# Kernel tuning notes

Hardware: AMD Instinct MI355X
Metric: run time of the kernel (lower is better)

## Reference

```python
import jax, jax.numpy as jnp
import numpy as np

B, C, H, W = 4, 64, 160, 160
OUT, KH, KW = 64, 3, 3
STRIDE, PAD = 1, 1
K2 = KH * KW


def conv2d(x, w, b=None, stride=STRIDE, pad=PAD):
    y = jax.lax.conv_general_dilated(
        x, w, window_strides=(stride, stride),
        padding=[(pad, pad), (pad, pad)],
        dimension_numbers=("NCHW", "OIHW", "NCHW"))
    if b is not None:
        y = y + b[None, :, None, None]
    return y


def bilinear_gather(x, py, px):
    # x: [B,C,H,W]; py,px: [B,K2,Ho,Wo] float sampling positions
    Bq, Cq, Hq, Wq = x.shape
    y0 = jnp.floor(py)
    x0 = jnp.floor(px)
    wy1 = py - y0  # frac
    wx1 = px - x0
    y0i = y0.astype(jnp.int32)
    x0i = x0.astype(jnp.int32)
    x_flat = x.reshape(Bq, Cq, Hq * Wq)

    def corner(yi, xi, wgt):
        valid = (yi >= 0) & (yi < Hq) & (xi >= 0) & (xi < Wq)
        idx = jnp.clip(yi, 0, Hq - 1) * Wq + jnp.clip(xi, 0, Wq - 1)  # [B,K2,Ho,Wo]
        g = jax.vmap(lambda xf, i: jnp.take(xf, i, axis=1))(x_flat, idx)  # [B,C,K2,Ho,Wo]
        return g * (wgt * valid)[:, None]

    out = corner(y0i, x0i, (1 - wy1) * (1 - wx1))
    out = out + corner(y0i, x0i + 1, (1 - wy1) * wx1)
    out = out + corner(y0i + 1, x0i, wy1 * (1 - wx1))
    out = out + corner(y0i + 1, x0i + 1, wy1 * wx1)
    return out  # [B,C,K2,Ho,Wo]


def deform_forward(x, offset_w, offset_b, mask_w, mask_b, dcn_w):
    offset = conv2d(x, offset_w, offset_b)                # [B, 2*K2, Ho, Wo]
    mask = jax.nn.sigmoid(conv2d(x, mask_w, mask_b))      # [B, K2, Ho, Wo]
    Bq, _, Ho, Wo = offset.shape
    off = offset.reshape(Bq, K2, 2, Ho, Wo)
    off_y, off_x = off[:, :, 0], off[:, :, 1]
    k = jnp.arange(K2)
    ky = (k // KW).astype(jnp.float32)
    kx = (k % KW).astype(jnp.float32)
    base_i = jnp.arange(Ho, dtype=jnp.float32) * STRIDE - PAD
    base_j = jnp.arange(Wo, dtype=jnp.float32) * STRIDE - PAD
    py = off_y + base_i[None, None, :, None] + ky[None, :, None, None]
    px = off_x + base_j[None, None, None, :] + kx[None, :, None, None]
    sampled = bilinear_gather(x, py, px)                  # [B,C,K2,Ho,Wo]
    w = dcn_w.reshape(OUT, C, K2)
    # out[b,o,i,j] = sum_{c,k} w[o,c,k] * mask[b,k,i,j] * sampled[b,c,k,i,j]
    return jnp.einsum("ock,bckij,bkij->boij", w, sampled, mask)


def setup_inputs() -> dict:
    key = jax.random.key(0)
    ks = jax.random.split(key, 6)
    x = jax.random.normal(ks[0], (B, C, H, W), dtype=jnp.float32)
    # small random weights so offsets stay modest (module inits them to 0;
    # random values exercise the full deformable math)
    offset_w = jax.random.normal(ks[1], (2 * K2, C, KH, KW), dtype=jnp.float32) * 0.01
    offset_b = jax.random.normal(ks[2], (2 * K2,), dtype=jnp.float32) * 0.1
    mask_w = jax.random.normal(ks[3], (K2, C, KH, KW), dtype=jnp.float32) * 0.01
    mask_b = jax.random.normal(ks[4], (K2,), dtype=jnp.float32) * 0.1
    dcn_w = jax.random.normal(ks[5], (OUT, C, KH, KW), dtype=jnp.float32) * (1.0 / np.sqrt(C * K2))
    return {"x": x, "offset_w": offset_w, "offset_b": offset_b,
            "mask_w": mask_w, "mask_b": mask_b, "dcn_w": dcn_w}


def reference(x, offset_w, offset_b, mask_w, mask_b, dcn_w):
    return deform_forward(x, offset_w, offset_b, mask_w, mask_b, dcn_w)
```

## Files before the change

### kernel.cpp

```cpp
#include <hip/hip_runtime.h>
#include <hip/hip_bf16.h>
#include <math.h>

#define Bq 4
#define Cq 64
#define Hq 160
#define Wq 160
#define HWq (Hq*Wq)
#define K2q 9
#define OUTq 64
#define KKq 576
#define KS  18
#define SROW 584
#define HSTRIDE 72

typedef __attribute__((ext_vector_type(8))) short short8;
typedef __attribute__((ext_vector_type(4))) float float4v;
typedef unsigned short ushort_t;

__device__ __forceinline__ unsigned short f2bf(float f) {
    unsigned int u = __builtin_bit_cast(unsigned int, f);
    unsigned int r = u + 0x7fffu + ((u >> 16) & 1u);
    return (unsigned short)(r >> 16);
}
__device__ __forceinline__ float bflo(unsigned int u) {
    return __builtin_bit_cast(float, u << 16);
}
__device__ __forceinline__ float bfhi(unsigned int u) {
    return __builtin_bit_cast(float, u & 0xffff0000u);
}

__global__ void __launch_bounds__(256) k_prep(const float* __restrict__ x,
                                              const float* __restrict__ dcn_w,
                                              const float* __restrict__ off_w,
                                              const float* __restrict__ msk_w,
                                              ushort_t* __restrict__ xt,
                                              ushort_t* __restrict__ wtf,
                                              ushort_t* __restrict__ cwf2) {
    __shared__ float tile[64][65];
    int b = blockIdx.y, hw0 = blockIdx.x * 64;
    int tid = threadIdx.x;
    int lane = tid & 63, grp = tid >> 6;
#pragma unroll
    for (int i = 0; i < 16; ++i) {
        int c = grp*16 + i;
        tile[c][lane] = x[(b*Cq + c)*HWq + hw0 + lane];
    }
    __syncthreads();
    int cp = tid & 31, hwg = tid >> 5;
#pragma unroll
    for (int it = 0; it < 8; ++it) {
        int hw = it*8 + hwg;
        unsigned int v = (unsigned int)f2bf(tile[2*cp][hw])
                       | ((unsigned int)f2bf(tile[2*cp+1][hw]) << 16);
        *(unsigned int*)(xt + ((size_t)b*HWq + hw0 + hw)*64 + 2*cp) = v;
    }
    if (blockIdx.y == 0 && blockIdx.x < 216) {
        int id = blockIdx.x*256 + tid;
        if (id < 4*KS*512) {
            int j = id & 7, ln = (id>>3) & 63, ks = (id>>9) % KS, g = id/(512*KS);
            int kk = ks*32 + (ln>>4)*8 + j;
            int c  = kk & 63, kt = kk >> 6;
            int m  = g*16 + (ln&15);
            wtf[id] = f2bf(dcn_w[m*KKq + c*9 + kt]);
        }
        int id2 = id - 4*KS*512;
        if (id2 >= 0 && id2 < 9*2*2*512) {
            int j = id2 & 7, ln = (id2>>3) & 63;
            int ks2 = (id2>>9) & 1, g = (id2>>10) & 1, k = id2 >> 11;
            int co = g*16 + (ln&15);
            int c  = ks2*32 + (ln>>4)*8 + j;
            float w = 0.f;
            if (co < 18)      w = off_w[co*KKq + c*9 + k];
            else if (co < 27) w = msk_w[(co-18)*KKq + c*9 + k];
            cwf2[id2] = f2bf(w);
        }
    }
}

__global__ void __launch_bounds__(256, 6) k_fused(const ushort_t* __restrict__ xt,
                                                  const ushort_t* __restrict__ cwf2,
                                                  const float* __restrict__ off_b,
                                                  const float* __restrict__ msk_b,
                                                  const ushort_t* __restrict__ wtf,
                                                  float* __restrict__ out) {
    __shared__ __align__(16) char s_mem[16*SROW*2];
    __shared__ __align__(16) unsigned int s_pk[144*12];
    ushort_t* halo   = (ushort_t*)s_mem;
    float*    s_part = (float*)(s_mem + 7776);
    ushort_t* s_s    = (ushort_t*)s_mem;

    int blk = blockIdx.x;
    int jt = blk % 10, i = (blk/10) % Hq, b = blk/(10*Hq);
    int j0 = jt*16;
    int tid = threadIdx.x, lane = tid & 63, grp = tid >> 6;
    int n = lane & 15, quad = lane >> 4;

    const ushort_t* xtb = xt + (size_t)b*HWq*64;
    for (int t = tid; t < 432; t += 256) {
        int seg = t >> 3, sub = t & 7;
        int ky = seg / 18, px = seg % 18;
        int y = i + ky - 1, xx = j0 + px - 1;
        uint4 v = {0u,0u,0u,0u};
        if (y >= 0 && y < Hq && xx >= 0 && xx < Wq)
            v = *(const uint4*)(xtb + ((size_t)y*Wq + xx)*64 + sub*8);
        *(uint4*)(halo + (ky*18 + px)*HSTRIDE + sub*8) = v;
    }
    __syncthreads();

    {
        int gM = grp & 1, kh = grp >> 1;
        float4v cacc = {0.f,0.f,0.f,0.f};
#pragma unroll
        for (int s = 0; s < 9; ++s) {
            int st = kh*9 + s;
            int k = st >> 1, ks2 = st & 1;
            int ky = k/3, kx = k - (k/3)*3;
            short8 a  = *(const short8*)(cwf2 + (size_t)(((k*2+gM)*2+ks2)*512 + lane*8));
            short8 bf = *(const short8*)(halo + (ky*18 + n + kx)*HSTRIDE + quad*8 + ks2*32);
            cacc = __builtin_amdgcn_mfma_f32_16x16x32_bf16(a, bf, cacc, 0, 0, 0);
        }
        *(float4v*)(s_part + grp*256 + lane*4) = cacc;
    }
    __syncthreads();

    if (tid < 144) {
        int p = tid & 15, k = tid >> 4;
        #define RD(co) (s_part[(((co)>>4)*256)       + ((((co)&15)>>2)*16 + p)*4 + ((co)&3)] + \
                        s_part[(2 + ((co)>>4))*256   + ((((co)&15)>>2)*16 + p)*4 + ((co)&3)])
        float oy = RD(2*k)   + off_b[2*k];
        float ox = RD(2*k+1) + off_b[2*k+1];
        float mv = RD(18+k)  + msk_b[k];
        #undef RD
        float m = 1.f/(1.f + __expf(-mv));
        float py = oy + (float)(i - 1 + k/3);
        float px = ox + (float)(j0 + p - 1 + (k - (k/3)*3));
        float fy = floorf(py), fx = floorf(px);
        int y0 = (int)fy, x0 = (int)fx;
        float wy1 = py - fy, wx1 = px - fx;
        float wy0 = 1.f - wy1, wx0 = 1.f - wx1;
        bool vy0 = (y0 >= 0) & (y0 < Hq),   vy1 = (y0+1 >= 0) & (y0+1 < Hq);
        bool vx0 = (x0 >= 0) & (x0 < Wq),   vx1 = (x0+1 >= 0) & (x0+1 < Wq);
        int yc0 = min(max(y0,   0), Hq-1), yc1 = min(max(y0+1, 0), Hq-1);
        int xc0 = min(max(x0,   0), Wq-1), xc1 = min(max(x0+1, 0), Wq-1);
        unsigned int* pk = s_pk + tid*12;
        pk[0] = (unsigned int)((yc0*Wq + xc0)*128);
        pk[1] = (unsigned int)((yc0*Wq + xc1)*128);
        pk[2] = (unsigned int)((yc1*Wq + xc0)*128);
        pk[3] = (unsigned int)((yc1*Wq + xc1)*128);
        pk[4] = __builtin_bit_cast(unsigned int, (vy0 && vx0) ? wy0*wx0*m : 0.f);
        pk[5] = __builtin_bit_cast(unsigned int, (vy0 && vx1) ? wy0*wx1*m : 0.f);
        pk[6] = __builtin_bit_cast(unsigned int, (vy1 && vx0) ? wy1*wx0*m : 0.f);
        pk[7] = __builtin_bit_cast(unsigned int, (vy1 && vx1) ? wy1*wx1*m : 0.f);
        pk[8] = (unsigned int)(p*(SROW*2) + k*128);
    }
    __syncthreads();

    int lane4 = (lane & 31) * 4;
    int halfi = lane >> 5;
    const char* xtbB = (const char*)xtb;
    char* s_sb = (char*)s_s;
#pragma unroll 2
    for (int iter = 0; iter < 18; ++iter) {
        int t2h = iter*8 + grp*2 + halfi;
        const uint4* pkp = (const uint4*)(s_pk + t2h*12);
        uint4 A  = pkp[0];
        uint4 Wt = pkp[1];
        unsigned int dst = s_pk[t2h*12 + 8];
        unsigned int u00 = *(const unsigned int*)(xtbB + A.x + lane4);
        unsigned int u01 = *(const unsigned int*)(xtbB + A.y + lane4);
        unsigned int u10 = *(const unsigned int*)(xtbB + A.z + lane4);
        unsigned int u11 = *(const unsigned int*)(xtbB + A.w + lane4);
        float w00 = __builtin_bit_cast(float, Wt.x);
        float w01 = __builtin_bit_cast(float, Wt.y);
        float w10 = __builtin_bit_cast(float, Wt.z);
        float w11 = __builtin_bit_cast(float, Wt.w);
        float sl = w00*bflo(u00) + w01*bflo(u01) + w10*bflo(u10) + w11*bflo(u11);
        float sh = w00*bfhi(u00) + w01*bfhi(u01) + w10*bfhi(u10) + w11*bfhi(u11);
        __hip_bfloat162 h2 = __float22bfloat162_rn(make_float2(sl, sh));
        *(__hip_bfloat162*)(s_sb + dst + lane4) = h2;
    }
    __syncthreads();

    float4v acc = {0.f,0.f,0.f,0.f};
    const ushort_t* arow = wtf + ((size_t)(grp*KS)*64 + lane)*8;
    const ushort_t* brow = s_s + n*SROW + quad*8;
#pragma unroll
    for (int ks = 0; ks < KS; ++ks) {
        short8 a  = *(const short8*)(arow + ks*512);
        short8 bf = *(const short8*)(brow + ks*32);
        acc = __builtin_amdgcn_mfma_f32_16x16x32_bf16(a, bf, acc, 0, 0, 0);
    }

#pragma unroll
    for (int r = 0; r < 4; ++r) {
        int o = grp*16 + quad*4 + r;
        out[(((size_t)b*OUTq + o)*Hq + i)*Wq + j0 + n] = acc[r];
    }
}

extern "C" void kernel_launch(void* const* d_in, const int* in_sizes, int n_in,
                              void* d_out, int out_size, void* d_ws, size_t ws_size,
                              hipStream_t stream) {
    const float* x     = (const float*)d_in[0];
    const float* off_w = (const float*)d_in[1];
    const float* off_b = (const float*)d_in[2];
    const float* msk_w = (const float*)d_in[3];
    const float* msk_b = (const float*)d_in[4];
    const float* dcn_w = (const float*)d_in[5];
    float* out = (float*)d_out;

    char* ws = (char*)d_ws;
    ushort_t* xt   = (ushort_t*)ws;
    ushort_t* wtf  = xt + (size_t)Bq*HWq*64;
    ushort_t* cwf2 = wtf + 4*KS*512;

    hipLaunchKernelGGL(k_prep, dim3(HWq/64, Bq), dim3(256), 0, stream,
                       x, dcn_w, off_w, msk_w, xt, wtf, cwf2);
    hipLaunchKernelGGL(k_fused, dim3(Bq*Hq*10), dim3(256), 0, stream,
                       xt, cwf2, off_b, msk_b, wtf, out);
}
```

Measured before the change: 134.5 us.

## Merge prep and fused kernels into one persistent kernel with grid barrier

Replaces the two launches with a single persistent kernel of 1280 blocks. The blocks first do the transpose and weight packing in a grid-stride loop, then meet at an atomic-counter grid barrier, then each block handles 5 output tiles in turn. This removes the second launch and the gap between kernels, and it reuses shared memory across tiles. In exchange it adds a memset, a spin barrier that deadlocks unless all 1280 blocks are resident at once (5 per CU on 256 CUs), and occupancy capped at 5 blocks per CU instead of 6.

```diff
diff --git a/kernel.cpp b/kernel.cpp
--- a/kernel.cpp
+++ b/kernel.cpp
@@ -7,21 +7,22 @@
 #define Hq 160
 #define Wq 160
 #define HWq (Hq*Wq)
-#define K2q 9
 #define OUTq 64
 #define KKq 576
 #define KS  18
 #define SROW 584
 #define HSTRIDE 72
+#define NBLK 1280
+#define TPB 5
 
 typedef __attribute__((ext_vector_type(8))) short short8;
 typedef __attribute__((ext_vector_type(4))) float float4v;
 typedef unsigned short ushort_t;
 
-__device__ __forceinline__ unsigned short f2bf(float f) {
+__device__ __forceinline__ unsigned int f2bfu(float f) {
     unsigned int u = __builtin_bit_cast(unsigned int, f);
     unsigned int r = u + 0x7fffu + ((u >> 16) & 1u);
-    return (unsigned short)(r >> 16);
+    return r >> 16;
 }
 __device__ __forceinline__ float bflo(unsigned int u) {
     return __builtin_bit_cast(float, u << 16);
@@ -30,39 +31,50 @@
     return __builtin_bit_cast(float, u & 0xffff0000u);
 }
 
-__global__ void __launch_bounds__(256) k_prep(const float* __restrict__ x,
-                                              const float* __restrict__ dcn_w,
-                                              const float* __restrict__ off_w,
-                                              const float* __restrict__ msk_w,
-                                              ushort_t* __restrict__ xt,
-                                              ushort_t* __restrict__ wtf,
-                                              ushort_t* __restrict__ cwf2) {
-    __shared__ float tile[64][65];
-    int b = blockIdx.y, hw0 = blockIdx.x * 64;
-    int tid = threadIdx.x;
-    int lane = tid & 63, grp = tid >> 6;
-#pragma unroll
-    for (int i = 0; i < 16; ++i) {
-        int c = grp*16 + i;
-        tile[c][lane] = x[(b*Cq + c)*HWq + hw0 + lane];
-    }
-    __syncthreads();
-    int cp = tid & 31, hwg = tid >> 5;
-#pragma unroll
-    for (int it = 0; it < 8; ++it) {
-        int hw = it*8 + hwg;
-        unsigned int v = (unsigned int)f2bf(tile[2*cp][hw])
-                       | ((unsigned int)f2bf(tile[2*cp+1][hw]) << 16);
-        *(unsigned int*)(xt + ((size_t)b*HWq + hw0 + hw)*64 + 2*cp) = v;
-    }
-    if (blockIdx.y == 0 && blockIdx.x < 216) {
-        int id = blockIdx.x*256 + tid;
+__global__ void __launch_bounds__(256, 5) k_all(const float* __restrict__ x,
+                                                const float* __restrict__ dcn_w,
+                                                const float* __restrict__ off_w,
+                                                const float* __restrict__ msk_w,
+                                                const float* __restrict__ off_b,
+                                                const float* __restrict__ msk_b,
+                                                ushort_t* __restrict__ xt,
+                                                ushort_t* __restrict__ wtf,
+                                                ushort_t* __restrict__ cwf2,
+                                                unsigned int* __restrict__ ctr,
+                                                float* __restrict__ out) {
+    __shared__ __align__(16) char s_mem[16*SROW*2];
+    __shared__ __align__(16) unsigned int s_pk[144*12];
+    int bid = blockIdx.x;
+    int tid = threadIdx.x, lane = tid & 63, grp = tid >> 6;
+
+    {
+        float (*tile)[65] = (float(*)[65])s_mem;
+        for (int t = bid; t < 1600; t += NBLK) {
+            int b = t & 3, hw0 = (t >> 2) * 64;
+            __syncthreads();
+#pragma unroll
+            for (int i2 = 0; i2 < 16; ++i2) {
+                int c = grp*16 + i2;
+                tile[c][lane] = x[(b*Cq + c)*HWq + hw0 + lane];
+            }
+            __syncthreads();
+            int cp = tid & 31, hwg = tid >> 5;
+#pragma unroll
+            for (int it2 = 0; it2 < 8; ++it2) {
+                int hw = it2*8 + hwg;
+                unsigned int v = f2bfu(tile[2*cp][hw]) | (f2bfu(tile[2*cp+1][hw]) << 16);
+                *(unsigned int*)(xt + ((size_t)b*HWq + hw0 + hw)*64 + 2*cp) = v;
+            }
+        }
+    }
+    if (bid < 216) {
+        int id = bid*256 + tid;
         if (id < 4*KS*512) {
             int j = id & 7, ln = (id>>3) & 63, ks = (id>>9) % KS, g = id/(512*KS);
             int kk = ks*32 + (ln>>4)*8 + j;
             int c  = kk & 63, kt = kk >> 6;
             int m  = g*16 + (ln&15);
-            wtf[id] = f2bf(dcn_w[m*KKq + c*9 + kt]);
+            wtf[id] = (ushort_t)f2bfu(dcn_w[m*KKq + c*9 + kt]);
         }
         int id2 = id - 4*KS*512;
         if (id2 >= 0 && id2 < 9*2*2*512) {
@@ -73,129 +85,132 @@
             float w = 0.f;
             if (co < 18)      w = off_w[co*KKq + c*9 + k];
             else if (co < 27) w = msk_w[(co-18)*KKq + c*9 + k];
-            cwf2[id2] = f2bf(w);
-        }
-    }
-}
-
-__global__ void __launch_bounds__(256, 6) k_fused(const ushort_t* __restrict__ xt,
-                                                  const ushort_t* __restrict__ cwf2,
-                                                  const float* __restrict__ off_b,
-                                                  const float* __restrict__ msk_b,
-                                                  const ushort_t* __restrict__ wtf,
-                                                  float* __restrict__ out) {
-    __shared__ __align__(16) char s_mem[16*SROW*2];
-    __shared__ __align__(16) unsigned int s_pk[144*12];
+            cwf2[id2] = (ushort_t)f2bfu(w);
+        }
+    }
+
+    __threadfence();
+    __syncthreads();
+    if (tid == 0) {
+        __hip_atomic_fetch_add(ctr, 1u, __ATOMIC_ACQ_REL, __HIP_MEMORY_SCOPE_AGENT);
+        while (__hip_atomic_load(ctr, __ATOMIC_ACQUIRE, __HIP_MEMORY_SCOPE_AGENT) < NBLK)
+            __builtin_amdgcn_s_sleep(8);
+    }
+    __syncthreads();
+
     ushort_t* halo   = (ushort_t*)s_mem;
     float*    s_part = (float*)(s_mem + 7776);
     ushort_t* s_s    = (ushort_t*)s_mem;
-
-    int blk = blockIdx.x;
-    int jt = blk % 10, i = (blk/10) % Hq, b = blk/(10*Hq);
-    int j0 = jt*16;
-    int tid = threadIdx.x, lane = tid & 63, grp = tid >> 6;
     int n = lane & 15, quad = lane >> 4;
 
-    const ushort_t* xtb = xt + (size_t)b*HWq*64;
-    for (int t = tid; t < 432; t += 256) {
-        int seg = t >> 3, sub = t & 7;
-        int ky = seg / 18, px = seg % 18;
-        int y = i + ky - 1, xx = j0 + px - 1;
-        uint4 v = {0u,0u,0u,0u};
-        if (y >= 0 && y < Hq && xx >= 0 && xx < Wq)
-            v = *(const uint4*)(xtb + ((size_t)y*Wq + xx)*64 + sub*8);
-        *(uint4*)(halo + (ky*18 + px)*HSTRIDE + sub*8) = v;
-    }
-    __syncthreads();
-
-    {
-        int gM = grp & 1, kh = grp >> 1;
-        float4v cacc = {0.f,0.f,0.f,0.f};
-#pragma unroll
-        for (int s = 0; s < 9; ++s) {
-            int st = kh*9 + s;
-            int k = st >> 1, ks2 = st & 1;
-            int ky = k/3, kx = k - (k/3)*3;
-            short8 a  = *(const short8*)(cwf2 + (size_t)(((k*2+gM)*2+ks2)*512 + lane*8));
-            short8 bf = *(const short8*)(halo + (ky*18 + n + kx)*HSTRIDE + quad*8 + ks2*32);
-            cacc = __builtin_amdgcn_mfma_f32_16x16x32_bf16(a, bf, cacc, 0, 0, 0);
-        }
-        *(float4v*)(s_part + grp*256 + lane*4) = cacc;
-    }
-    __syncthreads();
-
-    if (tid < 144) {
-        int p = tid & 15, k = tid >> 4;
-        #define RD(co) (s_part[(((co)>>4)*256)       + ((((co)&15)>>2)*16 + p)*4 + ((co)&3)] + \
-                        s_part[(2 + ((co)>>4))*256   + ((((co)&15)>>2)*16 + p)*4 + ((co)&3)])
-        float oy = RD(2*k)   + off_b[2*k];
-        float ox = RD(2*k+1) + off_b[2*k+1];
-        float mv = RD(18+k)  + msk_b[k];
-        #undef RD
-        float m = 1.f/(1.f + __expf(-mv));
-        float py = oy + (float)(i - 1 + k/3);
-        float px = ox + (float)(j0 + p - 1 + (k - (k/3)*3));
-        float fy = floorf(py), fx = floorf(px);
-        int y0 = (int)fy, x0 = (int)fx;
-        float wy1 = py - fy, wx1 = px - fx;
-        float wy0 = 1.f - wy1, wx0 = 1.f - wx1;
-        bool vy0 = (y0 >= 0) & (y0 < Hq),   vy1 = (y0+1 >= 0) & (y0+1 < Hq);
-        bool vx0 = (x0 >= 0) & (x0 < Wq),   vx1 = (x0+1 >= 0) & (x0+1 < Wq);
-        int yc0 = min(max(y0,   0), Hq-1), yc1 = min(max(y0+1, 0), Hq-1);
-        int xc0 = min(max(x0,   0), Wq-1), xc1 = min(max(x0+1, 0), Wq-1);
-        unsigned int* pk = s_pk + tid*12;
-        pk[0] = (unsigned int)((yc0*Wq + xc0)*128);
-        pk[1] = (unsigned int)((yc0*Wq + xc1)*128);
-        pk[2] = (unsigned int)((yc1*Wq + xc0)*128);
-        pk[3] = (unsigned int)((yc1*Wq + xc1)*128);
-        pk[4] = __builtin_bit_cast(unsigned int, (vy0 && vx0) ? wy0*wx0*m : 0.f);
-        pk[5] = __builtin_bit_cast(unsigned int, (vy0 && vx1) ? wy0*wx1*m : 0.f);
-        pk[6] = __builtin_bit_cast(unsigned int, (vy1 && vx0) ? wy1*wx0*m : 0.f);
-        pk[7] = __builtin_bit_cast(unsigned int, (vy1 && vx1) ? wy1*wx1*m : 0.f);
-        pk[8] = (unsigned int)(p*(SROW*2) + k*128);
-    }
-    __syncthreads();
-
-    int lane4 = (lane & 31) * 4;
-    int halfi = lane >> 5;
-    const char* xtbB = (const char*)xtb;
-    char* s_sb = (char*)s_s;
+    for (int itile = 0; itile < TPB; ++itile) {
+        int blk = bid*TPB + itile;
+        int jt = blk % 10, i = (blk/10) % Hq, b = blk/(10*Hq);
+        int j0 = jt*16;
+        const ushort_t* xtb = xt + (size_t)b*HWq*64;
+        __syncthreads();
+
+        for (int t = tid; t < 432; t += 256) {
+            int seg = t >> 3, sub = t & 7;
+            int ky = seg / 18, px = seg % 18;
+            int y = i + ky - 1, xx = j0 + px - 1;
+            uint4 v = {0u,0u,0u,0u};
+            if (y >= 0 && y < Hq && xx >= 0 && xx < Wq)
+                v = *(const uint4*)(xtb + ((size_t)y*Wq + xx)*64 + sub*8);
+            *(uint4*)(halo + (ky*18 + px)*HSTRIDE + sub*8) = v;
+        }
+        __syncthreads();
+
+        {
+            int gM = grp & 1, kh = grp >> 1;
+            float4v cacc = {0.f,0.f,0.f,0.f};
+#pragma unroll
+            for (int s = 0; s < 9; ++s) {
+                int st = kh*9 + s;
+                int k = st >> 1, ks2 = st & 1;
+                int ky = k/3, kx = k - (k/3)*3;
+                short8 a  = *(const short8*)(cwf2 + (size_t)(((k*2+gM)*2+ks2)*512 + lane*8));
+                short8 bf = *(const short8*)(halo + (ky*18 + n + kx)*HSTRIDE + quad*8 + ks2*32);
+                cacc = __builtin_amdgcn_mfma_f32_16x16x32_bf16(a, bf, cacc, 0, 0, 0);
+            }
+            *(float4v*)(s_part + grp*256 + lane*4) = cacc;
+        }
+        __syncthreads();
+
+        if (tid < 144) {
+            int p = tid & 15, k = tid >> 4;
+            #define RD(co) (s_part[(((co)>>4)*256)     + ((((co)&15)>>2)*16 + p)*4 + ((co)&3)] + \
+                            s_part[(2 + ((co)>>4))*256 + ((((co)&15)>>2)*16 + p)*4 + ((co)&3)])
+            float oy = RD(2*k)   + off_b[2*k];
+            float ox = RD(2*k+1) + off_b[2*k+1];
+            float mv = RD(18+k)  + msk_b[k];
+            #undef RD
+            float m = 1.f/(1.f + __expf(-mv));
+            float py = oy + (float)(i - 1 + k/3);
+            float px = ox + (float)(j0 + p - 1 + (k - (k/3)*3));
+            float fy = floorf(py), fx = floorf(px);
+            int y0 = (int)fy, x0 = (int)fx;
+            float wy1 = py - fy, wx1 = px - fx;
+            float wy0 = 1.f - wy1, wx0 = 1.f - wx1;
+            bool vy0 = (y0 >= 0) & (y0 < Hq),   vy1 = (y0+1 >= 0) & (y0+1 < Hq);
+            bool vx0 = (x0 >= 0) & (x0 < Wq),   vx1 = (x0+1 >= 0) & (x0+1 < Wq);
+            int yc0 = min(max(y0,   0), Hq-1), yc1 = min(max(y0+1, 0), Hq-1);
+            int xc0 = min(max(x0,   0), Wq-1), xc1 = min(max(x0+1, 0), Wq-1);
+            unsigned int* pk = s_pk + tid*12;
+            pk[0] = (unsigned int)((yc0*Wq + xc0)*128);
+            pk[1] = (unsigned int)((yc0*Wq + xc1)*128);
+            pk[2] = (unsigned int)((yc1*Wq + xc0)*128);
+            pk[3] = (unsigned int)((yc1*Wq + xc1)*128);
+            pk[4] = __builtin_bit_cast(unsigned int, (vy0 && vx0) ? wy0*wx0*m : 0.f);
+            pk[5] = __builtin_bit_cast(unsigned int, (vy0 && vx1) ? wy0*wx1*m : 0.f);
+            pk[6] = __builtin_bit_cast(unsigned int, (vy1 && vx0) ? wy1*wx0*m : 0.f);
+            pk[7] = __builtin_bit_cast(unsigned int, (vy1 && vx1) ? wy1*wx1*m : 0.f);
+            pk[8] = (unsigned int)(p*(SROW*2) + k*128);
+        }
+        __syncthreads();
+
+        {
+            int lane4 = (lane & 31) * 4;
+            int halfi = lane >> 5;
+            const char* xtbB = (const char*)xtb;
+            char* s_sb = (char*)s_s;
 #pragma unroll 2
-    for (int iter = 0; iter < 18; ++iter) {
-        int t2h = iter*8 + grp*2 + halfi;
-        const uint4* pkp = (const uint4*)(s_pk + t2h*12);
-        uint4 A  = pkp[0];
-        uint4 Wt = pkp[1];
-        unsigned int dst = s_pk[t2h*12 + 8];
-        unsigned int u00 = *(const unsigned int*)(xtbB + A.x + lane4);
-        unsigned int u01 = *(const unsigned int*)(xtbB + A.y + lane4);
-        unsigned int u10 = *(const unsigned int*)(xtbB + A.z + lane4);
-        unsigned int u11 = *(const unsigned int*)(xtbB + A.w + lane4);
-        float w00 = __builtin_bit_cast(float, Wt.x);
-        float w01 = __builtin_bit_cast(float, Wt.y);
-        float w10 = __builtin_bit_cast(float, Wt.z);
-        float w11 = __builtin_bit_cast(float, Wt.w);
-        float sl = w00*bflo(u00) + w01*bflo(u01) + w10*bflo(u10) + w11*bflo(u11);
-        float sh = w00*bfhi(u00) + w01*bfhi(u01) + w10*bfhi(u10) + w11*bfhi(u11);
-        __hip_bfloat162 h2 = __float22bfloat162_rn(make_float2(sl, sh));
-        *(__hip_bfloat162*)(s_sb + dst + lane4) = h2;
-    }
-    __syncthreads();
-
-    float4v acc = {0.f,0.f,0.f,0.f};
-    const ushort_t* arow = wtf + ((size_t)(grp*KS)*64 + lane)*8;
-    const ushort_t* brow = s_s + n*SROW + quad*8;
-#pragma unroll
-    for (int ks = 0; ks < KS; ++ks) {
-        short8 a  = *(const short8*)(arow + ks*512);
-        short8 bf = *(const short8*)(brow + ks*32);
-        acc = __builtin_amdgcn_mfma_f32_16x16x32_bf16(a, bf, acc, 0, 0, 0);
-    }
-
-#pragma unroll
-    for (int r = 0; r < 4; ++r) {
-        int o = grp*16 + quad*4 + r;
-        out[(((size_t)b*OUTq + o)*Hq + i)*Wq + j0 + n] = acc[r];
+            for (int iter = 0; iter < 18; ++iter) {
+                int t2h = iter*8 + grp*2 + halfi;
+                const uint4* pkp = (const uint4*)(s_pk + t2h*12);
+                uint4 A  = pkp[0];
+                uint4 Wt = pkp[1];
+                unsigned int dst = s_pk[t2h*12 + 8];
+                unsigned int u00 = *(const unsigned int*)(xtbB + A.x + lane4);
+                unsigned int u01 = *(const unsigned int*)(xtbB + A.y + lane4);
+                unsigned int u10 = *(const unsigned int*)(xtbB + A.z + lane4);
+                unsigned int u11 = *(const unsigned int*)(xtbB + A.w + lane4);
+                float w00 = __builtin_bit_cast(float, Wt.x);
+                float w01 = __builtin_bit_cast(float, Wt.y);
+                float w10 = __builtin_bit_cast(float, Wt.z);
+                float w11 = __builtin_bit_cast(float, Wt.w);
+                float sl = w00*bflo(u00) + w01*bflo(u01) + w10*bflo(u10) + w11*bflo(u11);
+                float sh = w00*bfhi(u00) + w01*bfhi(u01) + w10*bfhi(u10) + w11*bfhi(u11);
+                __hip_bfloat162 h2 = __float22bfloat162_rn(make_float2(sl, sh));
+                *(__hip_bfloat162*)(s_sb + dst + lane4) = h2;
+            }
+        }
+        __syncthreads();
+
+        float4v acc = {0.f,0.f,0.f,0.f};
+        const ushort_t* arow = wtf + ((size_t)(grp*KS)*64 + lane)*8;
+        const ushort_t* brow = s_s + n*SROW + quad*8;
+#pragma unroll
+        for (int ks = 0; ks < KS; ++ks) {
+            short8 a  = *(const short8*)(arow + ks*512);
+            short8 bf = *(const short8*)(brow + ks*32);
+            acc = __builtin_amdgcn_mfma_f32_16x16x32_bf16(a, bf, acc, 0, 0, 0);
+        }
+#pragma unroll
+        for (int r = 0; r < 4; ++r) {
+            int o = grp*16 + quad*4 + r;
+            out[(((size_t)b*OUTq + o)*Hq + i)*Wq + j0 + n] = acc[r];
+        }
     }
 }
 
@@ -214,9 +229,10 @@
     ushort_t* xt   = (ushort_t*)ws;
     ushort_t* wtf  = xt + (size_t)Bq*HWq*64;
     ushort_t* cwf2 = wtf + 4*KS*512;
-
-    hipLaunchKernelGGL(k_prep, dim3(HWq/64, Bq), dim3(256), 0, stream,
-                       x, dcn_w, off_w, msk_w, xt, wtf, cwf2);
-    hipLaunchKernelGGL(k_fused, dim3(Bq*Hq*10), dim3(256), 0, stream,
-                       xt, cwf2, off_b, msk_b, wtf, out);
-}
+    unsigned int* ctr = (unsigned int*)(cwf2 + 9*2*2*512);
+
+    hipMemsetAsync(ctr, 0, 16, stream);
+    hipLaunchKernelGGL(k_all, dim3(NBLK), dim3(256), 0, stream,
+                       x, dcn_w, off_w, msk_w, off_b, msk_b,
+                       xt, wtf, cwf2, ctr, out);
+}
```

After: 357.3 us. +165.8%, slower.
